# Performance work log

Hardware: AMD Instinct MI355X
Metric: run time of the kernel (lower is better)

The kernel has to match this reference:

```python
import jax, jax.numpy as jnp
import numpy as np
from jax.ops import segment_sum, segment_max

N, F, D, E, G = 50000, 128, 64, 800000, 64
NEG_SLOPE = 0.2
EPS = 1e-16


def _glorot(key, shape):
    fan_in, fan_out = shape[0], shape[-1]
    lim = np.sqrt(6.0 / (fan_in + fan_out))
    return jax.random.uniform(key, shape, jnp.float32, -lim, lim)


def setup_inputs() -> dict:
    key = jax.random.key(0)
    ks = jax.random.split(key, 24)
    inp = {
        "x": jax.random.normal(ks[0], (N, F), jnp.float32),
        "edge_index": jax.random.randint(ks[1], (2, E), 0, N, jnp.int64),
        "batch": jnp.sort(jax.random.randint(ks[2], (N,), 0, G, jnp.int64)),
        "post_emb": jax.random.normal(ks[3], (G, D), jnp.float32),
    }
    in_dims = [F, D, D]
    for l in range(3):
        base = 4 + l * 5
        inp[f"Ws{l+1}"] = _glorot(ks[base + 0], (in_dims[l], D))
        inp[f"Wd{l+1}"] = _glorot(ks[base + 1], (in_dims[l], D))
        inp[f"as{l+1}"] = _glorot(ks[base + 2], (1, D))[0]
        inp[f"ad{l+1}"] = _glorot(ks[base + 3], (1, D))[0]
        inp[f"b{l+1}"] = jnp.zeros((D,), jnp.float32)
    inp["lin_w"] = _glorot(ks[20], (D, 2))
    inp["lin_b"] = jnp.zeros((2,), jnp.float32)
    return inp


def gat_layer(x, src, dst, Ws, Wd, a_s, a_d, b):
    xs = x @ Ws                      # [N, D] source-transformed features
    xd = x @ Wd                      # [N, D] dest-transformed features
    es = xs @ a_s                    # [N] per-node source attention logit
    ed = xd @ a_d                    # [N] per-node dest attention logit
    e = jax.nn.leaky_relu(es[src] + ed[dst], NEG_SLOPE)   # [E]
    m = segment_max(e, dst, num_segments=N)               # per-dest max
    p = jnp.exp(e - m[dst])
    z = segment_sum(p, dst, num_segments=N)
    alpha = p / (z[dst] + EPS)                            # softmax over in-edges
    out = segment_sum(alpha[:, None] * xs[src], dst, num_segments=N)
    return out + b


def reference(x, edge_index, batch, post_emb,
              Ws1, Wd1, as1, ad1, b1,
              Ws2, Wd2, as2, ad2, b2,
              Ws3, Wd3, as3, ad3, b3,
              lin_w, lin_b):
    src, dst = edge_index[0], edge_index[1]
    h = jax.nn.relu(gat_layer(x, src, dst, Ws1, Wd1, as1, ad1, b1))
    h = jax.nn.relu(gat_layer(h, src, dst, Ws2, Wd2, as2, ad2, b2))
    h = gat_layer(h, src, dst, Ws3, Wd3, as3, ad3, b3)
    # mean pooling per graph
    sums = segment_sum(h, batch, num_segments=G)
    cnt = segment_sum(jnp.ones((N,), h.dtype), batch, num_segments=G)
    pooled = sums / jnp.maximum(cnt, 1.0)[:, None]         # [G, D]
    z = jnp.concatenate([pooled, post_emb], axis=0)        # torch.concat dim=0
    return z @ lin_w + lin_b
```

## Files before the change

### kernel.cpp

```cpp
#include <hip/hip_runtime.h>
#include <hip/hip_fp16.h>
#include <math.h>

#define NN 50000
#define FF 128
#define DD 64
#define EE 800000
#define GG 64
#define NEG_SLOPE 0.2f
#define EPSV 1e-16f

#define NBKT 196
#define BCAP 5120
#define CHUNK 4096
#define NCH ((EE + CHUNK - 1) / CHUNK)


__global__ __launch_bounds__(256) void bin_k(const int* __restrict__ src,
                                             const int* __restrict__ dst,
                                             unsigned int* __restrict__ gbuf,
                                             int* __restrict__ gcur) {
    __shared__ unsigned int staged[CHUNK];
    __shared__ int bc[256], bs[256], rb[256];
    int tid = threadIdx.x;
    bc[tid] = 0;
    __syncthreads();
    int base = blockIdx.x * CHUNK;
    int cnt = min(CHUNK, EE - base);
    for (int i = tid; i < cnt; i += 256)
        atomicAdd(&bc[((unsigned)dst[base + i]) >> 8], 1);
    __syncthreads();
    int v = bc[tid];
    bs[tid] = v;
    __syncthreads();
    for (int off = 1; off < 256; off <<= 1) {
        int t = (tid >= off) ? bs[tid - off] : 0;
        __syncthreads();
        bs[tid] += t;
        __syncthreads();
    }
    int excl = bs[tid] - v;
    __syncthreads();
    bs[tid] = excl;
    bc[tid] = excl;
    rb[tid] = atomicAdd(&gcur[tid], v);
    __syncthreads();
    for (int i = tid; i < cnt; i += 256) {
        unsigned int d = (unsigned)dst[base + i];
        unsigned int s = (unsigned)src[base + i];
        int pos = atomicAdd(&bc[d >> 8], 1);
        staged[pos] = (s << 16) | d;
    }
    __syncthreads();
    for (int i = tid; i < cnt; i += 256) {
        unsigned int p = staged[i];
        int b = (int)((p & 0xFFFFu) >> 8);
        gbuf[(size_t)b * BCAP + rb[b] + (i - bs[b])] = p;
    }
}

__global__ void bpre_k(const int* __restrict__ gcur, int* __restrict__ bktoff,
                       int* __restrict__ rowstart) {
    __shared__ int s[256];
    int tid = threadIdx.x;
    int v = (tid < NBKT) ? gcur[tid] : 0;
    s[tid] = v;
    __syncthreads();
    for (int off = 1; off < 256; off <<= 1) {
        int t = (tid >= off) ? s[tid - off] : 0;
        __syncthreads();
        s[tid] += t;
        __syncthreads();
    }
    bktoff[tid] = s[tid] - v;
    if (tid == 0) rowstart[NN] = EE;
}

__global__ __launch_bounds__(256) void build_k(const unsigned int* __restrict__ gbuf,
                                               const int* __restrict__ gcur,
                                               const int* __restrict__ bktoff,
                                               int* __restrict__ rowstart,
                                               int* __restrict__ csr) {
    __shared__ unsigned int st[BCAP];
    __shared__ int hist[256], sc[256], cur[256];
    int tid = threadIdx.x, b = blockIdx.x;
    hist[tid] = 0;
    __syncthreads();
    int nb = gcur[b];
    const unsigned int* bb = gbuf + (size_t)b * BCAP;
    for (int i = tid; i < nb; i += 256) {
        unsigned int p = bb[i];
        st[i] = p;
        atomicAdd(&hist[p & 255u], 1);
    }
    __syncthreads();
    int v = hist[tid];
    sc[tid] = v;
    __syncthreads();
    for (int off = 1; off < 256; off <<= 1) {
        int t = (tid >= off) ? sc[tid - off] : 0;
        __syncthreads();
        sc[tid] += t;
        __syncthreads();
    }
    int rs = bktoff[b] + sc[tid] - v;
    int node = b * 256 + tid;
    if (node < NN) rowstart[node] = rs;
    cur[tid] = rs;
    __syncthreads();
    for (int i = tid; i < nb; i += 256) {
        unsigned int p = st[i];
        int pos = atomicAdd(&cur[p & 255u], 1);
        csr[pos] = (int)(p >> 16);
    }
}


__global__ void vecs3_k(const float* __restrict__ Wd0, const float* __restrict__ ad0,
                        const float* __restrict__ Ws0, const float* __restrict__ as0,
                        const float* __restrict__ Wd1, const float* __restrict__ ad1,
                        const float* __restrict__ Ws1, const float* __restrict__ as1,
                        const float* __restrict__ Wd2, const float* __restrict__ ad2,
                        const float* __restrict__ Ws2, const float* __restrict__ as2,
                        float* __restrict__ wdadAll, float* __restrict__ wsasAll) {
    int b = blockIdx.x;
    const float* Wd = (b == 0) ? Wd0 : (b == 1) ? Wd1 : Wd2;
    const float* ad = (b == 0) ? ad0 : (b == 1) ? ad1 : ad2;
    const float* Ws = (b == 0) ? Ws0 : (b == 1) ? Ws1 : Ws2;
    const float* as = (b == 0) ? as0 : (b == 1) ? as1 : as2;
    int Din = (b == 0) ? FF : DD;
    int k = threadIdx.x;
    if (k < Din) {
        float accd = 0.f, accs = 0.f;
        for (int d2 = 0; d2 < DD; ++d2) {
            accd += Wd[k * DD + d2] * ad[d2];
            accs += Ws[k * DD + d2] * as[d2];
        }
        wdadAll[b * FF + k] = accd;
        wsasAll[b * FF + k] = accs;
    }
}

template <int DIN, bool HIN>
__global__ __launch_bounds__(256, 4) void xform_k(
    const float* __restrict__ hf, const __half* __restrict__ hh,
    const float* __restrict__ Ws,
    const float* __restrict__ wsas, const float* __restrict__ wdad,
    __half* __restrict__ xs, float* __restrict__ es, float* __restrict__ ed,
    int n) {
    constexpr int PAD = DIN + 4;
    constexpr int XP = 68;
    __shared__ float hL[64 * PAD];
    int tid = threadIdx.x;
    int base = blockIdx.x * 64;

    {
        const int T4 = 64 * DIN / 4;
        int lim = n - base;
        lim = (lim > 64) ? T4 : lim * (DIN / 4);
        if constexpr (!HIN) {
            const float4* hg = reinterpret_cast<const float4*>(hf + (size_t)base * DIN);
            for (int i = tid; i < T4; i += 256) {
                float4 v = (i < lim) ? hg[i] : make_float4(0.f, 0.f, 0.f, 0.f);
                int r = i / (DIN / 4), c = i % (DIN / 4);
                *reinterpret_cast<float4*>(&hL[r * PAD + c * 4]) = v;
            }
        } else {
            const uint2* hg = reinterpret_cast<const uint2*>(hh + (size_t)base * DIN);
            for (int i = tid; i < T4; i += 256) {
                uint2 u = (i < lim) ? hg[i] : make_uint2(0u, 0u);
                float2 f01 = __half22float2(*reinterpret_cast<__half2*>(&u.x));
                float2 f23 = __half22float2(*reinterpret_cast<__half2*>(&u.y));
                int r = i / (DIN / 4), c = i % (DIN / 4);
                float* p = &hL[r * PAD + c * 4];
                p[0] = f01.x; p[1] = f01.y; p[2] = f23.x; p[3] = f23.y;
            }
        }
    }
    __syncthreads();

    int lane = tid & 63;
    int c0 = __builtin_amdgcn_readfirstlane((tid >> 6) << 4);
    float acc[16];
#pragma unroll
    for (int c = 0; c < 16; ++c) acc[c] = 0.f;
    float eacc = 0.f, dacc = 0.f;

    for (int k = 0; k < DIN; k += 4) {
        float4 hv = *reinterpret_cast<const float4*>(&hL[lane * PAD + k]);
        const float* w0 = Ws + (size_t)(k + 0) * DD + c0;
        const float* w1 = Ws + (size_t)(k + 1) * DD + c0;
        const float* w2 = Ws + (size_t)(k + 2) * DD + c0;
        const float* w3 = Ws + (size_t)(k + 3) * DD + c0;
#pragma unroll
        for (int c = 0; c < 16; ++c) {
            acc[c] = fmaf(hv.x, w0[c], acc[c]);
            acc[c] = fmaf(hv.y, w1[c], acc[c]);
            acc[c] = fmaf(hv.z, w2[c], acc[c]);
            acc[c] = fmaf(hv.w, w3[c], acc[c]);
        }
        eacc = fmaf(hv.x, wsas[k + 0], eacc); eacc = fmaf(hv.y, wsas[k + 1], eacc);
        eacc = fmaf(hv.z, wsas[k + 2], eacc); eacc = fmaf(hv.w, wsas[k + 3], eacc);
        dacc = fmaf(hv.x, wdad[k + 0], dacc); dacc = fmaf(hv.y, wdad[k + 1], dacc);
        dacc = fmaf(hv.z, wdad[k + 2], dacc); dacc = fmaf(hv.w, wdad[k + 3], dacc);
    }

    if ((tid >> 6) == 0 && base + lane < n) {
        es[base + lane] = eacc;
        ed[base + lane] = dacc;
    }
    __syncthreads();
    float* xsL = hL;
#pragma unroll
    for (int c = 0; c < 16; c += 4)
        *reinterpret_cast<float4*>(&xsL[lane * XP + c0 + c]) =
            make_float4(acc[c], acc[c + 1], acc[c + 2], acc[c + 3]);
    __syncthreads();
    {
        for (int i = tid; i < 64 * 16; i += 256) {
            int r = i >> 4, c4 = i & 15;
            if (base + r < n) {
                const float* f = &xsL[r * XP + c4 * 4];
                __half2 a = __floats2half2_rn(f[0], f[1]);
                __half2 b2 = __floats2half2_rn(f[2], f[3]);
                uint2 u;
                u.x = *reinterpret_cast<unsigned int*>(&a);
                u.y = *reinterpret_cast<unsigned int*>(&b2);
                *reinterpret_cast<uint2*>(xs + (size_t)(base + r) * DD + c4 * 4) = u;
            }
        }
    }
}

__global__ __launch_bounds__(256) void agg_k(
    const int* __restrict__ rowstart, const int* __restrict__ csr_src,
    const __half* __restrict__ xs, const float* __restrict__ es,
    const float* __restrict__ ed, const float* __restrict__ bias,
    __half* __restrict__ hout, int n, int relu) {
    int wid = (blockIdx.x * blockDim.x + threadIdx.x) >> 6;
    int lane = threadIdx.x & 63;
    if (wid >= n) return;
    int beg = rowstart[wid];
    int deg = rowstart[wid + 1] - beg;
    float edv = ed[wid];
    int slot = lane >> 3;
    int fl = lane & 7;

    float acc[8];
#pragma unroll
    for (int q = 0; q < 8; ++q) acc[q] = 0.f;
    float zl = 0.f;

    for (int c0 = 0; c0 < deg; c0 += 64) {
        int rem = min(64, deg - c0);
        int sv = 0;
        float pv = 0.f;
        if (lane < rem) {
            sv = csr_src[beg + c0 + lane];
            float e = es[sv] + edv;
            e = (e >= 0.f) ? e : NEG_SLOPE * e;
            pv = __expf(e);
        }
        zl += pv;
        int iters = (rem + 7) >> 3;
#pragma unroll 2
        for (int c = 0; c < iters; ++c) {
            int j = c * 8 + slot;
            float p = __shfl(pv, j, 64);
            int s = __shfl(sv, j, 64);
            uint4 u = *reinterpret_cast<const uint4*>(xs + (size_t)s * DD + fl * 8);
            unsigned int uu[4] = {u.x, u.y, u.z, u.w};
#pragma unroll
            for (int q = 0; q < 4; ++q) {
                float2 f = __half22float2(*reinterpret_cast<const __half2*>(&uu[q]));
                acc[2 * q]     = fmaf(p, f.x, acc[2 * q]);
                acc[2 * q + 1] = fmaf(p, f.y, acc[2 * q + 1]);
            }
        }
    }

#pragma unroll
    for (int off = 32; off; off >>= 1) zl += __shfl_xor(zl, off, 64);
#pragma unroll
    for (int q = 0; q < 8; ++q) {
        acc[q] += __shfl_xor(acc[q], 8, 64);
        acc[q] += __shfl_xor(acc[q], 16, 64);
        acc[q] += __shfl_xor(acc[q], 32, 64);
    }

    if (slot == 0) {
        float inv = 1.f / (zl + EPSV);
        const float4* bp = reinterpret_cast<const float4*>(bias) + fl * 2;
        float4 b0 = bp[0], b1 = bp[1];
        float v0 = fmaf(acc[0], inv, b0.x), v1 = fmaf(acc[1], inv, b0.y);
        float v2 = fmaf(acc[2], inv, b0.z), v3 = fmaf(acc[3], inv, b0.w);
        float v4 = fmaf(acc[4], inv, b1.x), v5 = fmaf(acc[5], inv, b1.y);
        float v6 = fmaf(acc[6], inv, b1.z), v7 = fmaf(acc[7], inv, b1.w);
        if (relu) {
            v0 = fmaxf(v0, 0.f); v1 = fmaxf(v1, 0.f);
            v2 = fmaxf(v2, 0.f); v3 = fmaxf(v3, 0.f);
            v4 = fmaxf(v4, 0.f); v5 = fmaxf(v5, 0.f);
            v6 = fmaxf(v6, 0.f); v7 = fmaxf(v7, 0.f);
        }
        __half2 h0 = __floats2half2_rn(v0, v1);
        __half2 h1 = __floats2half2_rn(v2, v3);
        __half2 h2 = __floats2half2_rn(v4, v5);
        __half2 h3 = __floats2half2_rn(v6, v7);
        uint4 u;
        u.x = *reinterpret_cast<unsigned int*>(&h0);
        u.y = *reinterpret_cast<unsigned int*>(&h1);
        u.z = *reinterpret_cast<unsigned int*>(&h2);
        u.w = *reinterpret_cast<unsigned int*>(&h3);
        *reinterpret_cast<uint4*>(hout + (size_t)wid * DD + fl * 8) = u;
    }
}


__global__ __launch_bounds__(256) void pool_k(
    const __half* __restrict__ h, const int* __restrict__ batch,
    float* __restrict__ psum, int n) {
    int wid = (blockIdx.x * blockDim.x + threadIdx.x) >> 6;
    int lane = threadIdx.x & 63;
    int beg = wid * 16;
    if (beg >= n) return;
    int end = min(beg + 16, n);
    int curg = batch[beg];
    float acc = 0.f;
    for (int i = beg; i < end; ++i) {
        int g = batch[i];
        if (g != curg) {
            atomicAdd(&psum[curg * DD + lane], acc);
            acc = 0.f; curg = g;
        }
        acc += __half2float(h[(size_t)i * DD + lane]);
    }
    atomicAdd(&psum[curg * DD + lane], acc);
}

__global__ void final_k(const float* __restrict__ psum, const int* __restrict__ batch,
                        const float* __restrict__ post_emb,
                        const float* __restrict__ lin_w, const float* __restrict__ lin_b,
                        float* __restrict__ out) {
    __shared__ int sL[GG + 1];
    int r = threadIdx.x;
    if (r <= GG) {
        int lo = 0, hi = NN;
        while (lo < hi) {
            int m = (lo + hi) >> 1;
            if (batch[m] < r) lo = m + 1; else hi = m;
        }
        sL[r] = lo;
    }
    __syncthreads();
    if (r >= 2 * GG) return;
    float o0 = 0.f, o1 = 0.f;
    if (r < GG) {
        float c = fmaxf((float)(sL[r + 1] - sL[r]), 1.f);
        float inv = 1.f / c;
        for (int d2 = 0; d2 < DD; ++d2) {
            float v = psum[r * DD + d2] * inv;
            o0 = fmaf(v, lin_w[d2 * 2 + 0], o0);
            o1 = fmaf(v, lin_w[d2 * 2 + 1], o1);
        }
    } else {
        const float* pe = post_emb + (size_t)(r - GG) * DD;
        for (int d2 = 0; d2 < DD; ++d2) {
            float v = pe[d2];
            o0 = fmaf(v, lin_w[d2 * 2 + 0], o0);
            o1 = fmaf(v, lin_w[d2 * 2 + 1], o1);
        }
    }
    out[r * 2 + 0] = o0 + lin_b[0];
    out[r * 2 + 1] = o1 + lin_b[1];
}


extern "C" void kernel_launch(void* const* d_in, const int* in_sizes, int n_in,
                              void* d_out, int out_size, void* d_ws, size_t ws_size,
                              hipStream_t stream) {
    const float* x        = (const float*)d_in[0];
    const int*   ei       = (const int*)d_in[1];
    const int*   src      = ei;
    const int*   dst      = ei + EE;
    const int*   batch    = (const int*)d_in[2];
    const float* post_emb = (const float*)d_in[3];
    const float* Ws[3] = {(const float*)d_in[4],  (const float*)d_in[9],  (const float*)d_in[14]};
    const float* Wd[3] = {(const float*)d_in[5],  (const float*)d_in[10], (const float*)d_in[15]};
    const float* av[3] = {(const float*)d_in[6],  (const float*)d_in[11], (const float*)d_in[16]};
    const float* ad[3] = {(const float*)d_in[7],  (const float*)d_in[12], (const float*)d_in[17]};
    const float* bb[3] = {(const float*)d_in[8],  (const float*)d_in[13], (const float*)d_in[18]};
    const float* lin_w = (const float*)d_in[19];
    const float* lin_b = (const float*)d_in[20];
    float* outp = (float*)d_out;

    char* w = (char*)d_ws;
    size_t off = 0;
    auto alloc = [&](size_t bytes) -> char* {
        char* p = w + off;
        off += (bytes + 255) & ~(size_t)255;
        return p;
    };
    __half*       xs       = (__half*)alloc((size_t)NN * DD * 2);
    __half*       h16      = (__half*)alloc((size_t)NN * DD * 2);
    float*        es       = (float*)alloc((size_t)NN * 4);
    float*        ed       = (float*)alloc((size_t)NN * 4);
    int*          rowstart = (int*)alloc((size_t)(NN + 1) * 4);
    int*          csr      = (int*)alloc((size_t)EE * 4);
    float*        wdadAll  = (float*)alloc(3 * FF * 4);
    float*        wsasAll  = (float*)alloc(3 * FF * 4);
    float*        psum     = (float*)alloc((size_t)GG * DD * 4);
    unsigned int* gbuf     = (unsigned int*)alloc((size_t)NBKT * BCAP * 4);
    int*          gcur     = (int*)alloc(256 * 4);
    int*          bktoff   = (int*)alloc(256 * 4);

    hipMemsetAsync(gcur, 0, 256 * 4, stream);
    hipMemsetAsync(psum, 0, (size_t)GG * DD * 4, stream);
    bin_k<<<NCH, 256, 0, stream>>>(src, dst, gbuf, gcur);
    bpre_k<<<1, 256, 0, stream>>>(gcur, bktoff, rowstart);
    build_k<<<NBKT, 256, 0, stream>>>(gbuf, gcur, bktoff, rowstart, csr);

    vecs3_k<<<3, 128, 0, stream>>>(Wd[0], ad[0], Ws[0], av[0],
                                   Wd[1], ad[1], Ws[1], av[1],
                                   Wd[2], ad[2], Ws[2], av[2], wdadAll, wsasAll);

    const int XB = (NN + 63) / 64;
    for (int l = 0; l < 3; ++l) {
        if (l == 0)
            xform_k<FF, false><<<XB, 256, 0, stream>>>(x, nullptr, Ws[l],
                                                       wsasAll + l * FF, wdadAll + l * FF,
                                                       xs, es, ed, NN);
        else
            xform_k<DD, true><<<XB, 256, 0, stream>>>(nullptr, h16, Ws[l],
                                                      wsasAll + l * FF, wdadAll + l * FF,
                                                      xs, es, ed, NN);
        agg_k<<<(NN * 64 + 255) / 256, 256, 0, stream>>>(rowstart, csr, xs, es, ed,
                                                         bb[l], h16, NN, (l < 2) ? 1 : 0);
    }

    pool_k<<<((NN + 15) / 16 * 64 + 255) / 256, 256, 0, stream>>>(h16, batch, psum, NN);
    final_k<<<1, 128, 0, stream>>>(psum, batch, post_emb, lin_w, lin_b, outp);
}
```

Measured before the change: 187.0 us.

## Fold memsets and bucket prefix into fewer kernels; store CSR sources as uint16

```diff
diff --git a/kernel.cpp b/kernel.cpp
--- a/kernel.cpp
+++ b/kernel.cpp
@@ -14,6 +14,38 @@
 #define BCAP 5120
 #define CHUNK 4096
 #define NCH ((EE + CHUNK - 1) / CHUNK)
+
+__global__ __launch_bounds__(256) void init_k(
+    const float* __restrict__ Wd0, const float* __restrict__ ad0,
+    const float* __restrict__ Ws0, const float* __restrict__ as0,
+    const float* __restrict__ Wd1, const float* __restrict__ ad1,
+    const float* __restrict__ Ws1, const float* __restrict__ as1,
+    const float* __restrict__ Wd2, const float* __restrict__ ad2,
+    const float* __restrict__ Ws2, const float* __restrict__ as2,
+    float* __restrict__ wdadAll, float* __restrict__ wsasAll,
+    int* __restrict__ gcur, float* __restrict__ psum) {
+    int b = blockIdx.x;
+    int k = threadIdx.x;
+    if (b == 3) {
+        gcur[k] = 0;
+        for (int i = k; i < GG * DD; i += 256) psum[i] = 0.f;
+        return;
+    }
+    const float* Wd = (b == 0) ? Wd0 : (b == 1) ? Wd1 : Wd2;
+    const float* ad = (b == 0) ? ad0 : (b == 1) ? ad1 : ad2;
+    const float* Ws = (b == 0) ? Ws0 : (b == 1) ? Ws1 : Ws2;
+    const float* as = (b == 0) ? as0 : (b == 1) ? as1 : as2;
+    int Din = (b == 0) ? FF : DD;
+    if (k < Din) {
+        float accd = 0.f, accs = 0.f;
+        for (int d2 = 0; d2 < DD; ++d2) {
+            accd += Wd[k * DD + d2] * ad[d2];
+            accs += Ws[k * DD + d2] * as[d2];
+        }
+        wdadAll[b * FF + k] = accd;
+        wsasAll[b * FF + k] = accs;
+    }
+}
 
 
 __global__ __launch_bounds__(256) void bin_k(const int* __restrict__ src,
@@ -59,31 +91,27 @@
     }
 }
 
-__global__ void bpre_k(const int* __restrict__ gcur, int* __restrict__ bktoff,
-                       int* __restrict__ rowstart) {
-    __shared__ int s[256];
-    int tid = threadIdx.x;
-    int v = (tid < NBKT) ? gcur[tid] : 0;
-    s[tid] = v;
-    __syncthreads();
-    for (int off = 1; off < 256; off <<= 1) {
-        int t = (tid >= off) ? s[tid - off] : 0;
-        __syncthreads();
-        s[tid] += t;
-        __syncthreads();
-    }
-    bktoff[tid] = s[tid] - v;
-    if (tid == 0) rowstart[NN] = EE;
-}
-
 __global__ __launch_bounds__(256) void build_k(const unsigned int* __restrict__ gbuf,
                                                const int* __restrict__ gcur,
-                                               const int* __restrict__ bktoff,
                                                int* __restrict__ rowstart,
-                                               int* __restrict__ csr) {
+                                               unsigned short* __restrict__ csr) {
     __shared__ unsigned int st[BCAP];
     __shared__ int hist[256], sc[256], cur[256];
     int tid = threadIdx.x, b = blockIdx.x;
+
+    int gv = (tid < NBKT) ? gcur[tid] : 0;
+    sc[tid] = gv;
+    __syncthreads();
+    for (int off = 1; off < 256; off <<= 1) {
+        int t = (tid >= off) ? sc[tid - off] : 0;
+        __syncthreads();
+        sc[tid] += t;
+        __syncthreads();
+    }
+    int bktoff = sc[b] - gcur[b];
+    if (b == 0 && tid == 0) rowstart[NN] = EE;
+    __syncthreads();
+
     hist[tid] = 0;
     __syncthreads();
     int nb = gcur[b];
@@ -103,7 +131,7 @@
         sc[tid] += t;
         __syncthreads();
     }
-    int rs = bktoff[b] + sc[tid] - v;
+    int rs = bktoff + sc[tid] - v;
     int node = b * 256 + tid;
     if (node < NN) rowstart[node] = rs;
     cur[tid] = rs;
@@ -111,35 +139,10 @@
     for (int i = tid; i < nb; i += 256) {
         unsigned int p = st[i];
         int pos = atomicAdd(&cur[p & 255u], 1);
-        csr[pos] = (int)(p >> 16);
-    }
-}
-
-
-__global__ void vecs3_k(const float* __restrict__ Wd0, const float* __restrict__ ad0,
-                        const float* __restrict__ Ws0, const float* __restrict__ as0,
-                        const float* __restrict__ Wd1, const float* __restrict__ ad1,
-                        const float* __restrict__ Ws1, const float* __restrict__ as1,
-                        const float* __restrict__ Wd2, const float* __restrict__ ad2,
-                        const float* __restrict__ Ws2, const float* __restrict__ as2,
-                        float* __restrict__ wdadAll, float* __restrict__ wsasAll) {
-    int b = blockIdx.x;
-    const float* Wd = (b == 0) ? Wd0 : (b == 1) ? Wd1 : Wd2;
-    const float* ad = (b == 0) ? ad0 : (b == 1) ? ad1 : ad2;
-    const float* Ws = (b == 0) ? Ws0 : (b == 1) ? Ws1 : Ws2;
-    const float* as = (b == 0) ? as0 : (b == 1) ? as1 : as2;
-    int Din = (b == 0) ? FF : DD;
-    int k = threadIdx.x;
-    if (k < Din) {
-        float accd = 0.f, accs = 0.f;
-        for (int d2 = 0; d2 < DD; ++d2) {
-            accd += Wd[k * DD + d2] * ad[d2];
-            accs += Ws[k * DD + d2] * as[d2];
-        }
-        wdadAll[b * FF + k] = accd;
-        wsasAll[b * FF + k] = accs;
-    }
-}
+        csr[pos] = (unsigned short)(p >> 16);
+    }
+}
+
 
 template <int DIN, bool HIN>
 __global__ __launch_bounds__(256, 4) void xform_k(
@@ -233,7 +236,7 @@
 }
 
 __global__ __launch_bounds__(256) void agg_k(
-    const int* __restrict__ rowstart, const int* __restrict__ csr_src,
+    const int* __restrict__ rowstart, const unsigned short* __restrict__ csr_src,
     const __half* __restrict__ xs, const float* __restrict__ es,
     const float* __restrict__ ed, const float* __restrict__ bias,
     __half* __restrict__ hout, int n, int relu) {
@@ -256,7 +259,7 @@
         int sv = 0;
         float pv = 0.f;
         if (lane < rem) {
-            sv = csr_src[beg + c0 + lane];
+            sv = (int)csr_src[beg + c0 + lane];
             float e = es[sv] + edv;
             e = (e >= 0.f) ? e : NEG_SLOPE * e;
             pv = __expf(e);
@@ -400,28 +403,25 @@
         off += (bytes + 255) & ~(size_t)255;
         return p;
     };
-    __half*       xs       = (__half*)alloc((size_t)NN * DD * 2);
-    __half*       h16      = (__half*)alloc((size_t)NN * DD * 2);
-    float*        es       = (float*)alloc((size_t)NN * 4);
-    float*        ed       = (float*)alloc((size_t)NN * 4);
-    int*          rowstart = (int*)alloc((size_t)(NN + 1) * 4);
-    int*          csr      = (int*)alloc((size_t)EE * 4);
-    float*        wdadAll  = (float*)alloc(3 * FF * 4);
-    float*        wsasAll  = (float*)alloc(3 * FF * 4);
-    float*        psum     = (float*)alloc((size_t)GG * DD * 4);
-    unsigned int* gbuf     = (unsigned int*)alloc((size_t)NBKT * BCAP * 4);
-    int*          gcur     = (int*)alloc(256 * 4);
-    int*          bktoff   = (int*)alloc(256 * 4);
-
-    hipMemsetAsync(gcur, 0, 256 * 4, stream);
-    hipMemsetAsync(psum, 0, (size_t)GG * DD * 4, stream);
+    __half*         xs       = (__half*)alloc((size_t)NN * DD * 2);
+    __half*         h16      = (__half*)alloc((size_t)NN * DD * 2);
+    float*          es       = (float*)alloc((size_t)NN * 4);
+    float*          ed       = (float*)alloc((size_t)NN * 4);
+    int*            rowstart = (int*)alloc((size_t)(NN + 1) * 4);
+    unsigned short* csr      = (unsigned short*)alloc((size_t)EE * 2);
+    float*          wdadAll  = (float*)alloc(3 * FF * 4);
+    float*          wsasAll  = (float*)alloc(3 * FF * 4);
+    float*          psum     = (float*)alloc((size_t)GG * DD * 4);
+    unsigned int*   gbuf     = (unsigned int*)alloc((size_t)NBKT * BCAP * 4);
+    int*            gcur     = (int*)alloc(256 * 4);
+
+    init_k<<<4, 256, 0, stream>>>(Wd[0], ad[0], Ws[0], av[0],
+                                  Wd[1], ad[1], Ws[1], av[1],
+                                  Wd[2], ad[2], Ws[2], av[2],
+                                  wdadAll, wsasAll, gcur, psum);
+
     bin_k<<<NCH, 256, 0, stream>>>(src, dst, gbuf, gcur);
-    bpre_k<<<1, 256, 0, stream>>>(gcur, bktoff, rowstart);
-    build_k<<<NBKT, 256, 0, stream>>>(gbuf, gcur, bktoff, rowstart, csr);
-
-    vecs3_k<<<3, 128, 0, stream>>>(Wd[0], ad[0], Ws[0], av[0],
-                                   Wd[1], ad[1], Ws[1], av[1],
-                                   Wd[2], ad[2], Ws[2], av[2], wdadAll, wsasAll);
+    build_k<<<NBKT, 256, 0, stream>>>(gbuf, gcur, rowstart, csr);
 
     const int XB = (NN + 63) / 64;
     for (int l = 0; l < 3; ++l) {
```

Result: faster. 179.1 us (-4.2%).
